# Performance work log

Measured on AMD Instinct MI355X. Metric: run time of the kernel, lower is better.

## Reference

```python
import jax, jax.numpy as jnp
import numpy as np

EPS = 1e-7  # keras backend epsilon used inside K.ctc_decode's log


def setup_inputs() -> dict:
    key = jax.random.key(0)
    B, T, C = 64, 256, 2500
    logits = jax.random.normal(key, (B, T, C), dtype=jnp.float32)
    # K.ctc_decode expects softmax probabilities as input
    inputs = jax.nn.softmax(logits, axis=-1)
    return {"inputs": inputs}


def reference(inputs):
    """CTC best-path decode (beam_width=1), matching K.ctc_decode semantics:
    - log(probs + eps)
    - per-frame argmax, merge consecutive repeats, remove blank (= C-1)
    - dense output padded with -1, shape [B, T]
    - score = -(sum over frames of max log-prob), shape [B, 1]
    """
    B, T, C = inputs.shape
    blank = C - 1
    logp = jnp.log(inputs + EPS)                      # [B, T, C]
    best = jnp.argmax(logp, axis=-1)                  # [B, T] int
    max_lp = jnp.max(logp, axis=-1)                   # [B, T]

    # collapse: drop tokens equal to previous frame's token, then drop blanks
    prev = jnp.concatenate(
        [jnp.full((B, 1), -1, dtype=best.dtype), best[:, :-1]], axis=1
    )
    keep = (best != blank) & (best != prev)           # [B, T] bool

    # left-compact kept tokens into a -1 padded buffer (extra trash column T)
    pos = jnp.cumsum(keep.astype(jnp.int32), axis=1) - 1   # [B, T]
    pos = jnp.where(keep, pos, T)
    out = jnp.full((B, T + 1), -1, dtype=jnp.int32)
    batch_idx = jnp.arange(B)[:, None]
    out = out.at[batch_idx, pos].set(best.astype(jnp.int32))
    decoded = out[:, :T]                              # [B, T], -1 padded

    scores = -jnp.sum(max_lp, axis=1, keepdims=True)  # [B, 1]
    return decoded, scores
```

## Files before the change

kernel.cpp:

```cpp
#include <hip/hip_runtime.h>
#include <math.h>

#define BATCH 64
#define TLEN  256
#define NCLS  2500
#define BLANK (NCLS - 1)
#define EPSF  1e-7f
#define NF4   (NCLS / 4)
#define FULL_IT 9
#define TAIL_LANES (NF4 - FULL_IT * 64)

typedef float f32x4 __attribute__((ext_vector_type(4)));

__global__ __launch_bounds__(256) void ctc_rowmax_kernel(
    const float* __restrict__ in, int2* __restrict__ bml) {
  const int wid  = threadIdx.x >> 6;
  const int lane = threadIdx.x & 63;
  const int row  = (blockIdx.x << 2) + wid;
  const f32x4* __restrict__ p4 = (const f32x4*)(in + (size_t)row * NCLS) + lane;

  f32x4 v[FULL_IT + 1];
  #pragma unroll
  for (int it = 0; it < FULL_IT; ++it) v[it] = __builtin_nontemporal_load(p4 + (it << 6));
  const bool tail = lane < TAIL_LANES;
  if (tail) v[FULL_IT] = __builtin_nontemporal_load(p4 + (FULL_IT << 6));

  float vmax = -1.0f;
  int   vidx = 0;
  #pragma unroll
  for (int it = 0; it < FULL_IT; ++it) {
    const int base = (it << 8) + (lane << 2);
    if (v[it].x > vmax) { vmax = v[it].x; vidx = base;     }
    if (v[it].y > vmax) { vmax = v[it].y; vidx = base + 1; }
    if (v[it].z > vmax) { vmax = v[it].z; vidx = base + 2; }
    if (v[it].w > vmax) { vmax = v[it].w; vidx = base + 3; }
  }
  if (tail) {
    const int base = (FULL_IT << 8) + (lane << 2);
    if (v[FULL_IT].x > vmax) { vmax = v[FULL_IT].x; vidx = base;     }
    if (v[FULL_IT].y > vmax) { vmax = v[FULL_IT].y; vidx = base + 1; }
    if (v[FULL_IT].z > vmax) { vmax = v[FULL_IT].z; vidx = base + 2; }
    if (v[FULL_IT].w > vmax) { vmax = v[FULL_IT].w; vidx = base + 3; }
  }

  for (int off = 32; off > 0; off >>= 1) {
    float ov = __shfl_down(vmax, off);
    int   oi = __shfl_down(vidx, off);
    if (ov > vmax || (ov == vmax && oi < vidx)) { vmax = ov; vidx = oi; }
  }
  if (lane == 0) bml[row] = make_int2(vidx, __float_as_int(logf(vmax + EPSF)));
}

__global__ __launch_bounds__(256) void ctc_decode_kernel(
    const int2* __restrict__ bml, float* __restrict__ dec, float* __restrict__ score) {
  const int b = blockIdx.x, t = threadIdx.x;
  const int lane = t & 63, wid = t >> 6;

  const int2 bm = bml[b * TLEN + t];
  const int   my  = bm.x;
  const float mlp = __int_as_float(bm.y);

  const int prevw = __shfl_up(my, 1);
  const int prev  = (t == 0) ? -1 : (lane == 0 ? bml[b * TLEN + t - 1].x : prevw);
  const int keep  = (my != BLANK && my != prev) ? 1 : 0;

  int x = keep;
  #pragma unroll
  for (int off = 1; off < 64; off <<= 1) {
    int y = __shfl_up(x, off);
    if (lane >= off) x += y;
  }
  __shared__ int   s_wsum[4];
  __shared__ float s_fsum[4];
  if (lane == 63) s_wsum[wid] = x;

  float s = mlp;
  #pragma unroll
  for (int off = 32; off > 0; off >>= 1) s += __shfl_down(s, off);
  if (lane == 0) s_fsum[wid] = s;
  __syncthreads();

  int offset = 0;
  #pragma unroll
  for (int w = 0; w < 4; ++w) offset += (w < wid) ? s_wsum[w] : 0;
  const int pos = offset + x - 1;

  dec[b * TLEN + t] = -1.0f;
  __syncthreads();
  if (keep) dec[b * TLEN + pos] = (float)my;

  if (t == 0) score[b] = -(s_fsum[0] + s_fsum[1] + s_fsum[2] + s_fsum[3]);
}

extern "C" void kernel_launch(void* const* d_in, const int* in_sizes, int n_in,
                              void* d_out, int out_size, void* d_ws, size_t ws_size,
                              hipStream_t stream) {
  const float* in = (const float*)d_in[0];
  float* out = (float*)d_out;
  int2* bml = (int2*)d_ws;

  ctc_rowmax_kernel<<<(BATCH * TLEN) / 4, 256, 0, stream>>>(in, bml);
  ctc_decode_kernel<<<BATCH, 256, 0, stream>>>(bml, out, out + BATCH * TLEN);
}
```

Before: 29.80 us.

## Fuse row-max and decode into one per-batch kernel with shared memory

Merges the argmax kernel and the collapse/decode kernel into one launch. Each batch gets a 1024-thread block whose 16 waves each process 16 rows, staging best indices and max log-probs in shared memory before the scan and scatter. This removes the second launch and the workspace round trip. The cost is only 64 blocks on a GPU with far more CUs, so the memory-bound read of about 164 MB may get much less parallelism and bandwidth.

```diff
diff --git a/kernel.cpp b/kernel.cpp
--- a/kernel.cpp
+++ b/kernel.cpp
@@ -9,87 +9,95 @@
 #define NF4   (NCLS / 4)
 #define FULL_IT 9
 #define TAIL_LANES (NF4 - FULL_IT * 64)
+#define ROWS_PER_WAVE 16
 
 typedef float f32x4 __attribute__((ext_vector_type(4)));
 
-__global__ __launch_bounds__(256) void ctc_rowmax_kernel(
-    const float* __restrict__ in, int2* __restrict__ bml) {
-  const int wid  = threadIdx.x >> 6;
+__global__ __launch_bounds__(1024) void ctc_batch_kernel(
+    const float* __restrict__ in, float* __restrict__ dec, float* __restrict__ score) {
+  const int b    = blockIdx.x;
+  const int wv   = threadIdx.x >> 6;
   const int lane = threadIdx.x & 63;
-  const int row  = (blockIdx.x << 2) + wid;
-  const f32x4* __restrict__ p4 = (const f32x4*)(in + (size_t)row * NCLS) + lane;
 
-  f32x4 v[FULL_IT + 1];
-  #pragma unroll
-  for (int it = 0; it < FULL_IT; ++it) v[it] = __builtin_nontemporal_load(p4 + (it << 6));
-  const bool tail = lane < TAIL_LANES;
-  if (tail) v[FULL_IT] = __builtin_nontemporal_load(p4 + (FULL_IT << 6));
+  __shared__ int   s_best[TLEN];
+  __shared__ float s_mlp[TLEN];
+  __shared__ int   s_wsum[4];
+  __shared__ float s_fsum[4];
 
-  float vmax = -1.0f;
-  int   vidx = 0;
-  #pragma unroll
-  for (int it = 0; it < FULL_IT; ++it) {
-    const int base = (it << 8) + (lane << 2);
-    if (v[it].x > vmax) { vmax = v[it].x; vidx = base;     }
-    if (v[it].y > vmax) { vmax = v[it].y; vidx = base + 1; }
-    if (v[it].z > vmax) { vmax = v[it].z; vidx = base + 2; }
-    if (v[it].w > vmax) { vmax = v[it].w; vidx = base + 3; }
-  }
-  if (tail) {
-    const int base = (FULL_IT << 8) + (lane << 2);
-    if (v[FULL_IT].x > vmax) { vmax = v[FULL_IT].x; vidx = base;     }
-    if (v[FULL_IT].y > vmax) { vmax = v[FULL_IT].y; vidx = base + 1; }
-    if (v[FULL_IT].z > vmax) { vmax = v[FULL_IT].z; vidx = base + 2; }
-    if (v[FULL_IT].w > vmax) { vmax = v[FULL_IT].w; vidx = base + 3; }
+  const float* __restrict__ bbase = in + (size_t)b * TLEN * NCLS;
+
+  for (int r = 0; r < ROWS_PER_WAVE; ++r) {
+    const int row = wv * ROWS_PER_WAVE + r;
+    const f32x4* __restrict__ p4 = (const f32x4*)(bbase + (size_t)row * NCLS) + lane;
+
+    f32x4 v[FULL_IT + 1];
+    #pragma unroll
+    for (int it = 0; it < FULL_IT; ++it) v[it] = __builtin_nontemporal_load(p4 + (it << 6));
+    const bool tail = lane < TAIL_LANES;
+    if (tail) v[FULL_IT] = __builtin_nontemporal_load(p4 + (FULL_IT << 6));
+
+    float vmax = -1.0f;
+    int   vidx = 0;
+    #pragma unroll
+    for (int it = 0; it < FULL_IT; ++it) {
+      const int base = (it << 8) + (lane << 2);
+      if (v[it].x > vmax) { vmax = v[it].x; vidx = base;     }
+      if (v[it].y > vmax) { vmax = v[it].y; vidx = base + 1; }
+      if (v[it].z > vmax) { vmax = v[it].z; vidx = base + 2; }
+      if (v[it].w > vmax) { vmax = v[it].w; vidx = base + 3; }
+    }
+    if (tail) {
+      const int base = (FULL_IT << 8) + (lane << 2);
+      if (v[FULL_IT].x > vmax) { vmax = v[FULL_IT].x; vidx = base;     }
+      if (v[FULL_IT].y > vmax) { vmax = v[FULL_IT].y; vidx = base + 1; }
+      if (v[FULL_IT].z > vmax) { vmax = v[FULL_IT].z; vidx = base + 2; }
+      if (v[FULL_IT].w > vmax) { vmax = v[FULL_IT].w; vidx = base + 3; }
+    }
+    for (int off = 32; off > 0; off >>= 1) {
+      float ov = __shfl_down(vmax, off);
+      int   oi = __shfl_down(vidx, off);
+      if (ov > vmax || (ov == vmax && oi < vidx)) { vmax = ov; vidx = oi; }
+    }
+    if (lane == 0) { s_best[row] = vidx; s_mlp[row] = logf(vmax + EPSF); }
   }
 
-  for (int off = 32; off > 0; off >>= 1) {
-    float ov = __shfl_down(vmax, off);
-    int   oi = __shfl_down(vidx, off);
-    if (ov > vmax || (ov == vmax && oi < vidx)) { vmax = ov; vidx = oi; }
-  }
-  if (lane == 0) bml[row] = make_int2(vidx, __float_as_int(logf(vmax + EPSF)));
-}
-
-__global__ __launch_bounds__(256) void ctc_decode_kernel(
-    const int2* __restrict__ bml, float* __restrict__ dec, float* __restrict__ score) {
-  const int b = blockIdx.x, t = threadIdx.x;
-  const int lane = t & 63, wid = t >> 6;
-
-  const int2 bm = bml[b * TLEN + t];
-  const int   my  = bm.x;
-  const float mlp = __int_as_float(bm.y);
-
-  const int prevw = __shfl_up(my, 1);
-  const int prev  = (t == 0) ? -1 : (lane == 0 ? bml[b * TLEN + t - 1].x : prevw);
-  const int keep  = (my != BLANK && my != prev) ? 1 : 0;
-
-  int x = keep;
-  #pragma unroll
-  for (int off = 1; off < 64; off <<= 1) {
-    int y = __shfl_up(x, off);
-    if (lane >= off) x += y;
-  }
-  __shared__ int   s_wsum[4];
-  __shared__ float s_fsum[4];
-  if (lane == 63) s_wsum[wid] = x;
-
-  float s = mlp;
-  #pragma unroll
-  for (int off = 32; off > 0; off >>= 1) s += __shfl_down(s, off);
-  if (lane == 0) s_fsum[wid] = s;
   __syncthreads();
 
-  int offset = 0;
-  #pragma unroll
-  for (int w = 0; w < 4; ++w) offset += (w < wid) ? s_wsum[w] : 0;
-  const int pos = offset + x - 1;
+  const int t = threadIdx.x;
+  int my = 0, keep = 0, x = 0;
+  if (t < TLEN) {
+    my = s_best[t];
+    const int prev = (t == 0) ? -1 : s_best[t - 1];
+    keep = (my != BLANK && my != prev) ? 1 : 0;
 
-  dec[b * TLEN + t] = -1.0f;
+    x = keep;
+    #pragma unroll
+    for (int off = 1; off < 64; off <<= 1) {
+      int y = __shfl_up(x, off);
+      if (lane >= off) x += y;
+    }
+    if (lane == 63) s_wsum[wv] = x;
+
+    float s = s_mlp[t];
+    #pragma unroll
+    for (int off = 32; off > 0; off >>= 1) s += __shfl_down(s, off);
+    if (lane == 0) s_fsum[wv] = s;
+  }
   __syncthreads();
-  if (keep) dec[b * TLEN + pos] = (float)my;
 
-  if (t == 0) score[b] = -(s_fsum[0] + s_fsum[1] + s_fsum[2] + s_fsum[3]);
+  int pos = 0;
+  if (t < TLEN) {
+    int offset = 0;
+    #pragma unroll
+    for (int w = 0; w < 4; ++w) offset += (w < wv) ? s_wsum[w] : 0;
+    pos = offset + x - 1;
+    dec[b * TLEN + t] = -1.0f;
+  }
+  __syncthreads();
+  if (t < TLEN) {
+    if (keep) dec[b * TLEN + pos] = (float)my;
+    if (t == 0) score[b] = -(s_fsum[0] + s_fsum[1] + s_fsum[2] + s_fsum[3]);
+  }
 }
 
 extern "C" void kernel_launch(void* const* d_in, const int* in_sizes, int n_in,
@@ -97,8 +105,5 @@
                               hipStream_t stream) {
   const float* in = (const float*)d_in[0];
   float* out = (float*)d_out;
-  int2* bml = (int2*)d_ws;
-
-  ctc_rowmax_kernel<<<(BATCH * TLEN) / 4, 256, 0, stream>>>(in, bml);
-  ctc_decode_kernel<<<BATCH, 256, 0, stream>>>(bml, out, out + BATCH * TLEN);
+  ctc_batch_kernel<<<BATCH, 1024, 0, stream>>>(in, out, out + BATCH * TLEN);
 }
```

Result: slower. 65.59 us (+120.1%).
